# Performance work log

Hardware: AMD Instinct MI355X
Metric: run time of the kernel (lower is better)

## Reference

```python
import jax, jax.numpy as jnp
import numpy as np
import math
from jax import lax

KPAD = 4  # padding for 9x9 depthwise conv (same spatial size)

def dwconv(x, w, b):
    # x: [B,C,H,W], w: [C,1,9,9] depthwise (groups=C), b: [C]
    y = lax.conv_general_dilated(
        x, w, window_strides=(1, 1), padding=[(KPAD, KPAD), (KPAD, KPAD)],
        dimension_numbers=("NCHW", "OIHW", "NCHW"), feature_group_count=x.shape[1])
    return y + b[None, :, None, None]

def channel_pos_encoding(c, h, w, dtype):
    # position over channels, frequencies over the flattened spatial dim
    hw = h * w
    position = jnp.arange(c, dtype=jnp.float32)[:, None]                  # [C,1]
    div_term = jnp.exp(jnp.arange(0, hw, 2, dtype=jnp.float32) * (-math.log(10000.0) / hw))  # [hw/2]
    ang = position * div_term                                             # [C,hw/2]
    pe = jnp.stack([jnp.sin(ang), jnp.cos(ang)], axis=-1).reshape(c, hw)  # interleave sin/cos
    return pe.reshape(c, h, w).astype(dtype)

def setup_inputs() -> dict:
    key = jax.random.key(0)
    ks = jax.random.split(key, 9)
    B, C, H, W = 4, 256, 128, 128
    x = jax.random.normal(ks[0], (B, C, H, W), dtype=jnp.float32)
    def wgt(k):
        return jax.random.normal(k, (C, 1, 9, 9), dtype=jnp.float32) * 0.1
    return {
        "x": x,
        "q_w": wgt(ks[1]), "q_b": jax.random.normal(ks[2], (C,), dtype=jnp.float32) * 0.1,
        "k_w": wgt(ks[3]), "k_b": jax.random.normal(ks[4], (C,), dtype=jnp.float32) * 0.1,
        "v_w": wgt(ks[5]), "v_b": jax.random.normal(ks[6], (C,), dtype=jnp.float32) * 0.1,
        "o_w": wgt(ks[7]), "o_b": jax.random.normal(ks[8], (C,), dtype=jnp.float32) * 0.1,
        "num_heads": 8,
    }

def reference(x, q_w, q_b, k_w, k_b, v_w, v_b, o_w, o_b, num_heads):
    b, c, h, w = x.shape
    hw = h * w
    d = hw // num_heads  # per-head spatial dim
    x = x + channel_pos_encoding(c, h, w, x.dtype)[None]
    q = dwconv(x, q_w, q_b).reshape(b, c, num_heads, d)  # [B,C,H,D]
    k = dwconv(x, k_w, k_b).reshape(b, c, num_heads, d)
    v = dwconv(x, v_w, v_b).reshape(b, c, num_heads, d)
    # channel-over-channel attention in fp32 (matches forced fp32 cast)
    qk = jnp.einsum("bqhd,bkhd->bhqk", q.astype(jnp.float32), k.astype(jnp.float32)) / math.sqrt(hw)
    attn = jax.nn.softmax(qk, axis=-1)
    a = jnp.einsum("bhqk,bkhd->bqhd", attn.astype(v.dtype), v).reshape(b, c, h, w)
    return dwconv(a, o_w, o_b)
```

## Files before the change

kernel.cpp:

```cpp
#include <hip/hip_runtime.h>
#include <hip/hip_bf16.h>
#include <math.h>

#define BB 4
#define CC 256
#define HH 128
#define WW 128
#define HWS (HH*WW)
#define NHEADS 8
#define DD (HWS/NHEADS)

typedef __attribute__((ext_vector_type(8))) short bf16x8;
typedef __attribute__((ext_vector_type(4))) float f32x4;
typedef __attribute__((ext_vector_type(2))) __fp16 h16x2;
typedef __attribute__((ext_vector_type(8))) __fp16 h16x8;

#define GLD_LDS(g, l) __builtin_amdgcn_global_load_lds( \
    (const __attribute__((address_space(1))) void*)(g),  \
    (__attribute__((address_space(3))) void*)(l), 16, 0, 0)

static __device__ __forceinline__ unsigned short f2bf(float f) {
    unsigned int u = __float_as_uint(f);
    unsigned int r = (u + 0x7FFFu + ((u >> 16) & 1u)) >> 16;
    return (unsigned short)r;
}
static __device__ __forceinline__ float b2f(unsigned short u) {
    return __uint_as_float((unsigned int)u << 16);
}
static __device__ __forceinline__ unsigned int pk2(float a, float b) {
    union { h16x2 h; unsigned int u; } x;
    x.h = __builtin_amdgcn_cvt_pkrtz(a, b);
    return x.u;
}

__global__ __launch_bounds__(256) void build_wt(
    const float* __restrict__ qw, const float* __restrict__ kw,
    const float* __restrict__ vw, unsigned short* __restrict__ wt)
{
    const int c = blockIdx.x, cv = blockIdx.y;
    const float* w = (cv == 0) ? qw : (cv == 1) ? kw : vw;
    unsigned short* dst = wt + ((size_t)c * 3 + cv) * 9 * 512;
    for (int idx = threadIdx.x; idx < 9 * 512; idx += 256) {
        const int ky   = idx >> 9;
        const int rem  = idx & 511;
        const int lane = rem >> 3, e = rem & 7;
        const int m = lane & 15;
        const int k = ((lane >> 4) << 3) + e;
        const int d = k - m;
        const float v = (d >= 0 && d <= 8) ? w[c * 81 + ky * 9 + d] : 0.0f;
        const __fp16 hv = (__fp16)v;
        unsigned short bits;
        __builtin_memcpy(&bits, &hv, 2);
        dst[idx] = bits;
    }
}

#define FOFF 27648
#define PE_COEF   (-1.1243088e-3f)
#define PE_RSTEP  (0.99887632f)
__global__ __launch_bounds__(512, 6) void conv9qkv(
    const float* __restrict__ in,
    const unsigned short* __restrict__ wt,
    const float* __restrict__ b0, const float* __restrict__ b1,
    const float* __restrict__ b2,
    unsigned short* __restrict__ o0, unsigned short* __restrict__ o1,
    unsigned short* __restrict__ o2)
{
    __shared__ alignas(16) char lds[FOFF + 21760];

    const int u    = ((blockIdx.x & 7) << 8) + (blockIdx.x >> 3);
    const int c    = u >> 3;
    const int bidx = (u >> 1) & 3;
    const int tc   = (u & 1) << 6;
    const int tid  = threadIdx.x;
    const int lane = tid & 63;
    const int wr   = tid >> 6;
    const int r16  = lane & 15;
    const int g    = lane >> 4;

    for (int f = wr; f < 27; f += 8) {
        const char* src = (const char*)wt + (((size_t)c * 27 + f) << 10) + (lane << 4);
        GLD_LDS(src, lds + (f << 10) + (lane << 4));
    }

    const float* xp = in + ((size_t)(bidx * CC + c) << 14);
    const float cf  = (float)c;

    #pragma unroll
    for (int it = 0; it < 3; ++it) {
        const int i = tid + (it << 9);
        if (i < 1360) {
            const int row = i / 10;
            const int c8  = i - row * 10;
            const int gy  = row - 4;
            const int gx  = tc + (c8 << 3) - 4;
            uint4 wv = make_uint4(0u, 0u, 0u, 0u);
            if (gy >= 0 && gy < HH) {
                const float* xr = xp + (gy << 7);
                if (gx >= 0 && gx + 7 < WW) {
                    const float4 a0 = *(const float4*)(xr + gx);
                    const float4 a1 = *(const float4*)(xr + gx + 4);
                    float dt = __expf(PE_COEF * (float)(((gy << 7) + gx) >> 1));
                    float s, cc;
                    __sincosf(cf * dt, &s, &cc);
                    wv.x = pk2(a0.x + s, a0.y + cc);
                    dt *= PE_RSTEP;
                    __sincosf(cf * dt, &s, &cc);
                    wv.y = pk2(a0.z + s, a0.w + cc);
                    dt *= PE_RSTEP;
                    __sincosf(cf * dt, &s, &cc);
                    wv.z = pk2(a1.x + s, a1.y + cc);
                    dt *= PE_RSTEP;
                    __sincosf(cf * dt, &s, &cc);
                    wv.w = pk2(a1.z + s, a1.w + cc);
                } else {
                    float vv[8];
                    #pragma unroll
                    for (int e = 0; e < 8; ++e) {
                        const int gxe = gx + e;
                        float xv = 0.f;
                        if (gxe >= 0 && gxe < WW) {
                            const int flat = (gy << 7) + gxe;
                            const float dt = __expf(PE_COEF * (float)(flat >> 1));
                            float s, cc;
                            __sincosf(cf * dt, &s, &cc);
                            xv = xr[gxe] + ((flat & 1) ? cc : s);
                        }
                        vv[e] = xv;
                    }
                    wv.x = pk2(vv[0], vv[1]); wv.y = pk2(vv[2], vv[3]);
                    wv.z = pk2(vv[4], vv[5]); wv.w = pk2(vv[6], vv[7]);
                }
            }
            int byte = row * 160 + (c8 << 4);
            byte ^= (row & 7) << 4;
            *(uint4*)(lds + FOFF + byte) = wv;
        }
    }
    __syncthreads();

    f32x4 acc[3][4];
    {
        const float bq = b0[c], bk = b1[c], bv = b2[c];
        #pragma unroll
        for (int xt = 0; xt < 4; ++xt) {
            acc[0][xt] = (f32x4){bq, bq, bq, bq};
            acc[1][xt] = (f32x4){bk, bk, bk, bk};
            acc[2][xt] = (f32x4){bv, bv, bv, bv};
        }
    }

    const int rowbase = (wr << 4) + r16;
    __builtin_amdgcn_s_setprio(1);
    for (int ky = 0; ky < 9; ++ky) {
        const int row = rowbase + ky;
        const int sx  = (row & 7) << 4;
        const int rb  = row * 160 + (g << 4);
        h16x8 a[4];
        #pragma unroll
        for (int xt = 0; xt < 4; ++xt)
            a[xt] = *(const h16x8*)(lds + FOFF + ((rb + (xt << 5)) ^ sx));
        #pragma unroll
        for (int cv = 0; cv < 3; ++cv) {
            const h16x8 tf = *(const h16x8*)(lds + ((cv * 9 + ky) << 10) + (lane << 4));
            #pragma unroll
            for (int xt = 0; xt < 4; ++xt)
                acc[cv][xt] = __builtin_amdgcn_mfma_f32_16x16x32_f16(
                    tf, a[xt], acc[cv][xt], 0, 0, 0);
        }
    }
    __builtin_amdgcn_s_setprio(0);

    unsigned short* const outs[3] = { o0, o1, o2 };
    const size_t base = (((size_t)(bidx * NHEADS + wr) * CC + c) << 11)
                      + ((size_t)r16 << 7) + tc + (g << 2);
    #pragma unroll
    for (int cv = 0; cv < 3; ++cv)
        #pragma unroll
        for (int xt = 0; xt < 4; ++xt) {
            ushort4 uo;
            uo.x = f2bf(acc[cv][xt][0]); uo.y = f2bf(acc[cv][xt][1]);
            uo.z = f2bf(acc[cv][xt][2]); uo.w = f2bf(acc[cv][xt][3]);
            *(ushort4*)(outs[cv] + base + (xt << 4)) = uo;
        }
}

#define OTILE 21760
__global__ __launch_bounds__(512, 8) void conv9o(
    const unsigned short* __restrict__ ain,
    const float* __restrict__ w, const float* __restrict__ b,
    float* __restrict__ out)
{
    __shared__ alignas(16) char lds[OTILE + 9216];
    __shared__ float lw[81];

    const int u    = ((blockIdx.x & 7) << 8) + (blockIdx.x >> 3);
    const int c    = u >> 3;
    const int bidx = (u >> 1) & 3;
    const int tc   = (u & 1) << 6;
    const int plane = bidx * CC + c;
    const int tid  = threadIdx.x;
    const int lane = tid & 63;
    const int wr   = tid >> 6;
    const int r16  = lane & 15;
    const int g    = lane >> 4;

    if (tid < 81) lw[tid] = w[c * 81 + tid];

    const unsigned short* ap = ain + ((size_t)plane << 14);

    #pragma unroll
    for (int it = 0; it < 3; ++it) {
        const int i = tid + (it << 9);
        if (i < 1360) {
            const int row = i / 10;
            const int c8  = i - row * 10;
            const int gy  = row - 4;
            const int gx  = tc + (c8 << 3) - 4;
            uint4 wv = make_uint4(0u, 0u, 0u, 0u);
            if (gy >= 0 && gy < HH) {
                const unsigned short* ar = ap + (gy << 7);
                if (gx >= 0 && gx + 7 < WW) {
                    const bf16x8 uu = *(const bf16x8*)(ar + gx);
                    wv.x = pk2(b2f((unsigned short)uu[0]), b2f((unsigned short)uu[1]));
                    wv.y = pk2(b2f((unsigned short)uu[2]), b2f((unsigned short)uu[3]));
                    wv.z = pk2(b2f((unsigned short)uu[4]), b2f((unsigned short)uu[5]));
                    wv.w = pk2(b2f((unsigned short)uu[6]), b2f((unsigned short)uu[7]));
                } else {
                    float vv[8];
                    #pragma unroll
                    for (int e = 0; e < 8; ++e) {
                        const int gxe = gx + e;
                        vv[e] = (gxe >= 0 && gxe < WW) ? b2f(ar[gxe]) : 0.f;
                    }
                    wv.x = pk2(vv[0], vv[1]); wv.y = pk2(vv[2], vv[3]);
                    wv.z = pk2(vv[4], vv[5]); wv.w = pk2(vv[6], vv[7]);
                }
            }
            int byte = row * 160 + (c8 << 4);
            byte ^= (row & 7) << 4;
            *(uint4*)(lds + byte) = wv;
        }
    }
    __syncthreads();

    if (tid < 256) {
        const int ln = tid >> 2, qq = tid & 3;
        const int m  = ln & 15;
        const int k0 = ((ln >> 4) << 3) + (qq << 1);
        const int d0 = k0 - m, d1 = k0 + 1 - m;
        #pragma unroll
        for (int ky = 0; ky < 9; ++ky) {
            const float f0 = (d0 >= 0 && d0 <= 8) ? lw[ky * 9 + d0] : 0.f;
            const float f1 = (d1 >= 0 && d1 <= 8) ? lw[ky * 9 + d1] : 0.f;
            *(unsigned int*)(lds + OTILE + (ky << 10) + (ln << 4) + (qq << 2)) = pk2(f0, f1);
        }
    }
    __syncthreads();

    const float bv = b[c];
    f32x4 acc[4];
    #pragma unroll
    for (int xt = 0; xt < 4; ++xt) acc[xt] = (f32x4){bv, bv, bv, bv};

    const int rowbase = (wr << 4) + r16;
    __builtin_amdgcn_s_setprio(1);
    for (int ky = 0; ky < 9; ++ky) {
        const int row = rowbase + ky;
        const int sx  = (row & 7) << 4;
        const int rb  = row * 160 + (g << 4);
        h16x8 a[4];
        #pragma unroll
        for (int xt = 0; xt < 4; ++xt)
            a[xt] = *(const h16x8*)(lds + ((rb + (xt << 5)) ^ sx));
        const h16x8 tf = *(const h16x8*)(lds + OTILE + (ky << 10) + (lane << 4));
        #pragma unroll
        for (int xt = 0; xt < 4; ++xt)
            acc[xt] = __builtin_amdgcn_mfma_f32_16x16x32_f16(tf, a[xt], acc[xt], 0, 0, 0);
    }
    __builtin_amdgcn_s_setprio(0);

    const int y = (wr << 4) + r16;
    float* orow = out + ((size_t)plane << 14) + ((size_t)y << 7) + tc + (g << 2);
    #pragma unroll
    for (int xt = 0; xt < 4; ++xt)
        *(f32x4*)(orow + (xt << 4)) = acc[xt];
}

__global__ __launch_bounds__(256) void gemm_qk(
    const unsigned short* __restrict__ Abuf, const unsigned short* __restrict__ Bbuf,
    float* __restrict__ Sout)
{
    constexpr int KT = 2048;

    __shared__ char lds[49152];

    const int tid = threadIdx.x;
    const int bh  = blockIdx.z;
    const int m0  = blockIdx.y << 7;
    const int n0  = blockIdx.x << 6;

    const unsigned short* Ab = Abuf + (size_t)bh * CC * KT + (size_t)m0 * KT;
    const unsigned short* Bb = Bbuf + (size_t)bh * CC * KT + (size_t)n0 * KT;

    const int lane = tid & 63;
    const int w    = tid >> 6;
    const int wm   = (w >> 1) << 6;
    const int wn   = (w & 1) << 5;
    const int r16  = lane & 15;
    const int g    = lane >> 4;

    const int trow = tid >> 3;
    const int slot = tid & 7;

    f32x4 acc[4][2] = {};

    auto stage = [&](int h, int kt) {
        const int kc = kt << 6;
        char* base = lds + h * 24576;
        #pragma unroll
        for (int i = 0; i < 4; ++i) {
            const int row = (i << 5) + trow;
            const int gs  = slot ^ (row & 7);
            GLD_LDS((const char*)(Ab + (size_t)row * KT + kc) + gs * 16,
                    base + (i << 12) + tid * 16);
        }
        #pragma unroll
        for (int i = 0; i < 2; ++i) {
            const int row = (i << 5) + trow;
            const int gs  = slot ^ (row & 7);
            GLD_LDS((const char*)(Bb + (size_t)row * KT + kc) + gs * 16,
                    base + 16384 + (i << 12) + tid * 16);
        }
    };

    stage(0, 0);
    __syncthreads();

    for (int kt = 0; kt < KT / 64; ++kt) {
        const int cur = kt & 1;
        if (kt + 1 < KT / 64) stage(cur ^ 1, kt + 1);
        const char* hb = lds + cur * 24576;
        #pragma unroll
        for (int kk = 0; kk < 2; ++kk) {
            bf16x8 af[4], bfr[2];
            #pragma unroll
            for (int mi = 0; mi < 4; ++mi) {
                const int row = wm + (mi << 4) + r16;
                af[mi] = *(const bf16x8*)(hb + row * 128 + ((((kk << 2) + g) ^ (row & 7)) << 4));
            }
            #pragma unroll
            for (int nj = 0; nj < 2; ++nj) {
                const int row = wn + (nj << 4) + r16;
                bfr[nj] = *(const bf16x8*)(hb + 16384 + row * 128 + ((((kk << 2) + g) ^ (row & 7)) << 4));
            }
            #pragma unroll
            for (int mi = 0; mi < 4; ++mi)
                #pragma unroll
                for (int nj = 0; nj < 2; ++nj)
                    acc[mi][nj] = __builtin_amdgcn_mfma_f32_16x16x32_bf16(af[mi], bfr[nj], acc[mi][nj], 0, 0, 0);
        }
        __syncthreads();
    }

    float* sp = Sout + (size_t)bh * 65536;
    #pragma unroll
    for (int mi = 0; mi < 4; ++mi)
        #pragma unroll
        for (int nj = 0; nj < 2; ++nj)
            #pragma unroll
            for (int j = 0; j < 4; ++j) {
                const int row = m0 + wm + (mi << 4) + (g << 2) + j;
                const int col = n0 + wn + (nj << 4) + r16;
                sp[(size_t)row * 256 + col] = acc[mi][nj][j] * 0.0078125f;
            }
}

__global__ __launch_bounds__(256) void softmax_kernel(
    const float* __restrict__ S, unsigned short* __restrict__ P)
{
    const int row  = (blockIdx.x << 2) + (threadIdx.x >> 6);
    const int lane = threadIdx.x & 63;
    const float4 vv = *(const float4*)(S + ((size_t)row << 8) + (lane << 2));
    float m = fmaxf(fmaxf(vv.x, vv.y), fmaxf(vv.z, vv.w));
    #pragma unroll
    for (int o = 32; o; o >>= 1) m = fmaxf(m, __shfl_xor(m, o, 64));
    const float e0 = __expf(vv.x - m), e1 = __expf(vv.y - m);
    const float e2 = __expf(vv.z - m), e3 = __expf(vv.w - m);
    float s = (e0 + e1) + (e2 + e3);
    #pragma unroll
    for (int o = 32; o; o >>= 1) s += __shfl_xor(s, o, 64);
    const float r = 1.0f / s;
    ushort4 u;
    u.x = f2bf(e0 * r); u.y = f2bf(e1 * r); u.z = f2bf(e2 * r); u.w = f2bf(e3 * r);
    *(ushort4*)(P + ((size_t)row << 8) + (lane << 2)) = u;
}

__global__ __launch_bounds__(256) void gemm_pv(
    const unsigned short* __restrict__ Pbuf, const unsigned short* __restrict__ vbuf,
    unsigned short* __restrict__ Ao)
{
    __shared__ alignas(16) char lds[49152];

    const int tid = threadIdx.x;
    const int bh  = blockIdx.z;
    const int m0  = blockIdx.y << 7;
    const int n0  = blockIdx.x << 6;

    const unsigned short* Ab = Pbuf + ((size_t)bh << 16) + ((size_t)m0 << 8);

    const int lane = tid & 63;
    const int w    = tid >> 6;
    const int wm   = (w >> 1) << 6;
    const int wn   = (w & 1) << 5;
    const int r16  = lane & 15;
    const int g    = lane >> 4;
    const int trow = tid >> 3;
    const int slot = tid & 7;

    {
        #pragma unroll
        for (int i = 0; i < 4; ++i) {
            const int row = (i << 5) + trow;
            const int gs  = slot ^ (row & 7);
            GLD_LDS((const char*)(Ab + (size_t)row * 256) + gs * 16,
                    lds + (i << 12) + tid * 16);
        }
    }

    {
        const unsigned short* Vb = vbuf + (size_t)bh * (CC * DD) + n0;
        const int rl = tid >> 2, q4 = tid & 3;
        #pragma unroll
        for (int p = 0; p < 4; ++p) {
            const int cp = (p << 6) + rl;
            const unsigned short* src = Vb + (size_t)cp * DD + (q4 << 4);
            const bf16x8 v0 = *(const bf16x8*)(src);
            const bf16x8 v1 = *(const bf16x8*)(src + 8);
            const int cb = cp << 1;
            #pragma unroll
            for (int e = 0; e < 8; ++e) {
                const int d0 = (q4 << 4) + e, d1 = d0 + 8;
                *(unsigned short*)(lds + 16384 + d0 * 512 +
                    (cb ^ (((d0 & 7) ^ (d0 >> 3)) << 4))) = (unsigned short)v0[e];
                *(unsigned short*)(lds + 16384 + d1 * 512 +
                    (cb ^ (((d1 & 7) ^ (d1 >> 3)) << 4))) = (unsigned short)v1[e];
            }
        }
    }
    __syncthreads();

    f32x4 acc[4][2] = {};

    for (int kt = 0; kt < 4; ++kt) {
        #pragma unroll
        for (int kk = 0; kk < 2; ++kk) {
            bf16x8 af[4], bfr[2];
            #pragma unroll
            for (int mi = 0; mi < 4; ++mi) {
                const int row = wm + (mi << 4) + r16;
                af[mi] = *(const bf16x8*)(lds + row * 128 + ((((kk << 2) + g) ^ (row & 7)) << 4));
            }
            #pragma unroll
            for (int nj = 0; nj < 2; ++nj) {
                const int d = wn + (nj << 4) + r16;
                const int kbyte = (kt << 7) + ((((kk << 2) + g)) << 4);
                bfr[nj] = *(const bf16x8*)(lds + 16384 + d * 512 +
                    (kbyte ^ (((d & 7) ^ (d >> 3)) << 4)));
            }
            #pragma unroll
            for (int mi = 0; mi < 4; ++mi)
                #pragma unroll
                for (int nj = 0; nj < 2; ++nj)
                    acc[mi][nj] = __builtin_amdgcn_mfma_f32_16x16x32_bf16(af[mi], bfr[nj], acc[mi][nj], 0, 0, 0);
        }
        if (kt < 3) {
            __syncthreads();
            const int kc = (kt + 1) << 6;
            #pragma unroll
            for (int i = 0; i < 4; ++i) {
                const int row = (i << 5) + trow;
                const int gs  = slot ^ (row & 7);
                GLD_LDS((const char*)(Ab + (size_t)row * 256 + kc) + gs * 16,
                        lds + (i << 12) + tid * 16);
            }
            __syncthreads();
        }
    }

    const int b = bh >> 3, h = bh & 7;
    #pragma unroll
    for (int mi = 0; mi < 4; ++mi)
        #pragma unroll
        for (int nj = 0; nj < 2; ++nj)
            #pragma unroll
            for (int j = 0; j < 4; ++j) {
                const int row = m0 + wm + (mi << 4) + (g << 2) + j;
                const int col = n0 + wn + (nj << 4) + r16;
                Ao[((size_t)b * CC + row) * HWS + h * DD + col] = f2bf(acc[mi][nj][j]);
            }
}

extern "C" void kernel_launch(void* const* d_in, const int* in_sizes, int n_in,
                              void* d_out, int out_size, void* d_ws, size_t ws_size,
                              hipStream_t stream)
{
    const float* x  = (const float*)d_in[0];
    const float* qw = (const float*)d_in[1];
    const float* qb = (const float*)d_in[2];
    const float* kw = (const float*)d_in[3];
    const float* kb = (const float*)d_in[4];
    const float* vw = (const float*)d_in[5];
    const float* vb = (const float*)d_in[6];
    const float* ow = (const float*)d_in[7];
    const float* ob = (const float*)d_in[8];
    float* out = (float*)d_out;

    char* wsb = (char*)d_ws;
    __hip_bfloat16* q   = (__hip_bfloat16*)(wsb + 16777216UL);
    __hip_bfloat16* k   = (__hip_bfloat16*)(wsb + 50331648UL);
    float*          S   = (float*)(wsb + 83886080UL);
    __hip_bfloat16* P   = (__hip_bfloat16*)(wsb + 92274688UL);
    __hip_bfloat16* v   = (__hip_bfloat16*)(wsb + 96468992UL);
    unsigned short* A   = (unsigned short*)(wsb + 0);
    unsigned short* wt  = (unsigned short*)(wsb + 83886080UL);

    build_wt<<<dim3(CC, 3), 256, 0, stream>>>(qw, kw, vw, wt);
    conv9qkv<<<dim3(CC * 8), 512, 0, stream>>>(
        x, wt, qb, kb, vb,
        (unsigned short*)q, (unsigned short*)k, (unsigned short*)v);
    gemm_qk<<<dim3(4, 2, 32), 256, 0, stream>>>(
        (const unsigned short*)q, (const unsigned short*)k, S);
    softmax_kernel<<<dim3(2048), 256, 0, stream>>>(S, (unsigned short*)P);
    gemm_pv<<<dim3(32, 2, 32), 256, 0, stream>>>(
        (const unsigned short*)P, (const unsigned short*)v, A);
    conv9o<<<dim3(CC * 8), 512, 0, stream>>>(A, ow, ob, out);
}
```

Measured before the change: 143.1 us.

## Fuse Toeplitz weight build into QKV conv kernel and shrink LDS footprint

Removes the separate build_wt launch and instead builds the fp16 banded (Toeplitz) filter tiles directly in LDS inside conv9qkv from the raw fp32 weights. The all-zero fourth lane group is redirected to a shared zero row, which cuts filter storage from 1024 to 768 bytes per tile. The input tile drops from 10 to 9 columns and loses its XOR swizzle. Together these shrink LDS enough to raise the occupancy hint from 6 to 8 blocks. The trade-offs are more LDS bank conflicts without the swizzle, and scattered global weight reads repeated in every block.

```diff
diff --git a/kernel.cpp b/kernel.cpp
--- a/kernel.cpp
+++ b/kernel.cpp
@@ -33,40 +33,20 @@
     return x.u;
 }
 
-__global__ __launch_bounds__(256) void build_wt(
-    const float* __restrict__ qw, const float* __restrict__ kw,
-    const float* __restrict__ vw, unsigned short* __restrict__ wt)
-{
-    const int c = blockIdx.x, cv = blockIdx.y;
-    const float* w = (cv == 0) ? qw : (cv == 1) ? kw : vw;
-    unsigned short* dst = wt + ((size_t)c * 3 + cv) * 9 * 512;
-    for (int idx = threadIdx.x; idx < 9 * 512; idx += 256) {
-        const int ky   = idx >> 9;
-        const int rem  = idx & 511;
-        const int lane = rem >> 3, e = rem & 7;
-        const int m = lane & 15;
-        const int k = ((lane >> 4) << 3) + e;
-        const int d = k - m;
-        const float v = (d >= 0 && d <= 8) ? w[c * 81 + ky * 9 + d] : 0.0f;
-        const __fp16 hv = (__fp16)v;
-        unsigned short bits;
-        __builtin_memcpy(&bits, &hv, 2);
-        dst[idx] = bits;
-    }
-}
-
-#define FOFF 27648
+#define QZERO 20736
+#define QTILE 20992
 #define PE_COEF   (-1.1243088e-3f)
 #define PE_RSTEP  (0.99887632f)
-__global__ __launch_bounds__(512, 6) void conv9qkv(
+__global__ __launch_bounds__(512, 8) void conv9qkv(
     const float* __restrict__ in,
-    const unsigned short* __restrict__ wt,
+    const float* __restrict__ qw, const float* __restrict__ kw,
+    const float* __restrict__ vw,
     const float* __restrict__ b0, const float* __restrict__ b1,
     const float* __restrict__ b2,
     unsigned short* __restrict__ o0, unsigned short* __restrict__ o1,
     unsigned short* __restrict__ o2)
 {
-    __shared__ alignas(16) char lds[FOFF + 21760];
+    __shared__ alignas(16) char lds[40592];
 
     const int u    = ((blockIdx.x & 7) << 8) + (blockIdx.x >> 3);
     const int c    = u >> 3;
@@ -78,9 +58,32 @@
     const int r16  = lane & 15;
     const int g    = lane >> 4;
 
-    for (int f = wr; f < 27; f += 8) {
-        const char* src = (const char*)wt + (((size_t)c * 27 + f) << 10) + (lane << 4);
-        GLD_LDS(src, lds + (f << 10) + (lane << 4));
+    if (tid < 64) *(unsigned int*)(lds + QZERO + (tid << 2)) = 0u;
+    if (tid == 64) *(uint4*)(lds + QTILE + 19584) = make_uint4(0u, 0u, 0u, 0u);
+
+    {
+        const int qq  = tid & 3;
+        const int ln  = (tid >> 2) & 63;
+        const int grp = tid >> 8;
+        if (ln < 48) {
+            const int m  = ln & 15;
+            const int k0 = ((ln >> 4) << 3) + (qq << 1);
+            const int d0 = k0 - m, d1 = k0 + 1 - m;
+            const float* const ws[3] = { qw + c * 81, kw + c * 81, vw + c * 81 };
+            #pragma unroll
+            for (int cv = 0; cv < 3; ++cv) {
+                #pragma unroll
+                for (int kyi = 0; kyi < 5; ++kyi) {
+                    const int ky = grp + (kyi << 1);
+                    if (ky < 9) {
+                        const float f0 = (d0 >= 0 && d0 <= 8) ? ws[cv][ky * 9 + d0] : 0.f;
+                        const float f1 = (d1 >= 0 && d1 <= 8) ? ws[cv][ky * 9 + d1] : 0.f;
+                        *(unsigned int*)(lds + (cv * 9 + ky) * 768 + (ln << 4) + (qq << 2))
+                            = pk2(f0, f1);
+                    }
+                }
+            }
+        }
     }
 
     const float* xp = in + ((size_t)(bidx * CC + c) << 14);
@@ -89,9 +92,9 @@
     #pragma unroll
     for (int it = 0; it < 3; ++it) {
         const int i = tid + (it << 9);
-        if (i < 1360) {
-            const int row = i / 10;
-            const int c8  = i - row * 10;
+        if (i < 1224) {
+            const int row = i / 9;
+            const int c8  = i - row * 9;
             const int gy  = row - 4;
             const int gx  = tc + (c8 << 3) - 4;
             uint4 wv = make_uint4(0u, 0u, 0u, 0u);
@@ -132,9 +135,7 @@
                     wv.z = pk2(vv[4], vv[5]); wv.w = pk2(vv[6], vv[7]);
                 }
             }
-            int byte = row * 160 + (c8 << 4);
-            byte ^= (row & 7) << 4;
-            *(uint4*)(lds + FOFF + byte) = wv;
+            *(uint4*)(lds + QTILE + row * 144 + (c8 << 4)) = wv;
         }
     }
     __syncthreads();
@@ -150,19 +151,22 @@
         }
     }
 
-    const int rowbase = (wr << 4) + r16;
+    const int  rowbase = (wr << 4) + r16;
+    const bool zl   = (lane >= 48);
+    const int  tfl  = lane << 4;
+    const int  zoff = QZERO + ((lane & 15) << 4);
     __builtin_amdgcn_s_setprio(1);
     for (int ky = 0; ky < 9; ++ky) {
         const int row = rowbase + ky;
-        const int sx  = (row & 7) << 4;
-        const int rb  = row * 160 + (g << 4);
+        const int rb  = QTILE + row * 144 + (g << 4);
         h16x8 a[4];
         #pragma unroll
         for (int xt = 0; xt < 4; ++xt)
-            a[xt] = *(const h16x8*)(lds + FOFF + ((rb + (xt << 5)) ^ sx));
+            a[xt] = *(const h16x8*)(lds + rb + (xt << 5));
         #pragma unroll
         for (int cv = 0; cv < 3; ++cv) {
-            const h16x8 tf = *(const h16x8*)(lds + ((cv * 9 + ky) << 10) + (lane << 4));
+            const int fb = (cv * 9 + ky) * 768;
+            const h16x8 tf = *(const h16x8*)(lds + (zl ? zoff : fb + tfl));
             #pragma unroll
             for (int xt = 0; xt < 4; ++xt)
                 acc[cv][xt] = __builtin_amdgcn_mfma_f32_16x16x32_f16(
@@ -523,11 +527,9 @@
     __hip_bfloat16* P   = (__hip_bfloat16*)(wsb + 92274688UL);
     __hip_bfloat16* v   = (__hip_bfloat16*)(wsb + 96468992UL);
     unsigned short* A   = (unsigned short*)(wsb + 0);
-    unsigned short* wt  = (unsigned short*)(wsb + 83886080UL);
-
-    build_wt<<<dim3(CC, 3), 256, 0, stream>>>(qw, kw, vw, wt);
+
     conv9qkv<<<dim3(CC * 8), 512, 0, stream>>>(
-        x, wt, qb, kb, vb,
+        x, qw, kw, vw, qb, kb, vb,
         (unsigned short*)q, (unsigned short*)k, (unsigned short*)v);
     gemm_qk<<<dim3(4, 2, 32), 256, 0, stream>>>(
         (const unsigned short*)q, (const unsigned short*)k, S);
```

New measurement: 297.6 us. 108% more time.
